# Kernel tuning notes

Measured on AMD Instinct MI355X. Metric: run time of the kernel, lower is better.

## Reference

```python
import jax, jax.numpy as jnp
import numpy as np
from jax import lax

B, G, Hh, Wn = 16, 30, 24, 862   # batch, num_group, block_len(patch_len), enc_in
PRE = G * Hh                      # 720 = configs.pre_train
RATES = (1, 2)                    # configs.dilation_rate
K = 3                             # deformable / ff kernel size


def conv2d(x, w, b, pad, dil=1):
    y = lax.conv_general_dilated(x, w, (1, 1), [(pad, pad), (pad, pad)],
                                 rhs_dilation=(dil, dil),
                                 dimension_numbers=('NCHW', 'OIHW', 'NCHW'))
    return y + b[None, :, None, None]


def bilinear_sample(x, py, px):
    # x [B,C,H,W]; py,px [B,K2,H,W] -> [B,C,K2,H,W]; zero padding outside bounds
    H, W = x.shape[2], x.shape[3]
    y0f = jnp.floor(py); x0f = jnp.floor(px)
    wy = py - y0f; wx = px - x0f
    y0 = y0f.astype(jnp.int32); x0 = x0f.astype(jnp.int32)

    def corner(yi, xi, wgt):
        m = ((yi >= 0) & (yi < H) & (xi >= 0) & (xi < W)).astype(x.dtype)
        yc = jnp.clip(yi, 0, H - 1); xc = jnp.clip(xi, 0, W - 1)
        v = jax.vmap(lambda xb, yb, xbi: xb[:, yb, xbi])(x, yc, xc)  # [B,C,K2,H,W]
        return v * (m * wgt)[:, None]

    return (corner(y0, x0, (1 - wy) * (1 - wx))
            + corner(y0, x0 + 1, (1 - wy) * wx)
            + corner(y0 + 1, x0, wy * (1 - wx))
            + corner(y0 + 1, x0 + 1, wy * wx))


def deform_conv(x, w_off, b_off, w_def, b_def, r):
    # torchvision-style deform_conv2d with 3x3 kernel, dilation r, same padding
    b, c, h, w = x.shape
    off = conv2d(x, w_off, b_off, pad=r, dil=r).reshape(b, K * K, 2, h, w)
    kg = np.stack(np.meshgrid(np.arange(K) - 1, np.arange(K) - 1, indexing='ij'), -1).reshape(-1, 2)
    py = off[:, :, 0] + jnp.arange(h, dtype=x.dtype)[None, None, :, None] \
         + jnp.asarray(kg[:, 0] * r, x.dtype)[None, :, None, None]
    px = off[:, :, 1] + jnp.arange(w, dtype=x.dtype)[None, None, None, :] \
         + jnp.asarray(kg[:, 1] * r, x.dtype)[None, :, None, None]
    sampled = bilinear_sample(x, py, px)  # [B,C,9,H,W]
    o = w_def.shape[0]
    return jnp.einsum('bikhw,oik->bohw', sampled, w_def.reshape(o, c, K * K)) \
           + b_def[None, :, None, None]


def forward(x_enc, W_bl, b_bl, W_off, b_off, W_def, b_def, W_ff, b_ff, W_proj, b_proj):
    b = x_enc.shape[0]
    # block_linear on channel(group) dim: permute(0,2,3,1) -> Linear(G,G) -> permute back
    group_inner = jnp.einsum('bghw,kg->bkhw', x_enc, W_bl) + b_bl[None, :, None, None]
    # Multi_Def_Conv: sum of deformable conv branches over dilation rates
    mul_def = deform_conv(x_enc, W_off[0], b_off[0], W_def[0], b_def[0], RATES[0])
    for ri in range(1, len(RATES)):
        mul_def = mul_def + deform_conv(x_enc, W_off[ri], b_off[ri], W_def[ri], b_def[ri], RATES[ri])
    # softmax-gated fusion
    repres = group_inner + group_inner * jax.nn.softmax(mul_def, axis=1)
    # ff = Conv2d(G,G,3,pad=1) + Dropout (identity at eval)
    repres = conv2d(repres, W_ff, b_ff, pad=1)
    all_fea = repres.reshape(b, G * Hh, Wn)          # [B, pre_train, n]
    # proj(all_fea.permute(0,2,1)).permute(0,2,1)
    return jnp.einsum('bpn,qp->bqn', all_fea, W_proj) + b_proj[None, :, None]


def setup_inputs() -> dict:
    key = jax.random.key(0)
    ks = jax.random.split(key, 6)
    R = len(RATES)
    f32 = jnp.float32
    return {
        'x_enc': jax.random.normal(ks[0], (B, G, Hh, Wn), f32),
        'W_bl': jax.random.normal(ks[1], (G, G), f32) / np.sqrt(G).astype(np.float32),
        'b_bl': jnp.zeros((G,), f32),
        'W_off': jax.random.normal(ks[2], (R, 2 * K * K, G, K, K), f32) * 0.01,
        'b_off': jnp.zeros((R, 2 * K * K), f32),
        'W_def': jax.random.normal(ks[3], (R, G, G, K, K), f32) / np.sqrt(G * K * K).astype(np.float32),
        'b_def': jnp.zeros((R, G), f32),
        'W_ff': jax.random.normal(ks[4], (G, G, K, K), f32) / np.sqrt(G * K * K).astype(np.float32),
        'b_ff': jnp.zeros((G,), f32),
        'W_proj': jax.random.normal(ks[5], (PRE, PRE), f32) / np.sqrt(PRE).astype(np.float32),
        'b_proj': jnp.zeros((PRE,), f32),
        'epoch': 0,
        'i': 0,
    }


def reference(x_enc, W_bl, b_bl, W_off, b_off, W_def, b_def, W_ff, b_ff, W_proj, b_proj, epoch, i):
    return forward(x_enc, W_bl, b_bl, W_off, b_off, W_def, b_def, W_ff, b_ff, W_proj, b_proj)
```

## Files before the change

kernel.cpp:

```cpp
#include <hip/hip_runtime.h>

#define Bz 16
#define Gc 30
#define Hs 24
#define Wd_ 862
#define HW (Hs*Wd_)
#define BHW (Bz*HW)
#define PREN 720

__device__ __forceinline__ int imin(int a,int b){return a<b?a:b;}
__device__ __forceinline__ int imax(int a,int b){return a>b?a:b;}

struct Corners { float m00,m01,m10,m11; int i00,i01,i10,i11; };

__device__ __forceinline__ Corners mk_corners(float py, float px){
  float y0f = floorf(py), x0f = floorf(px);
  float wy = py - y0f, wx = px - x0f;
  int y0 = (int)y0f, x0 = (int)x0f;
  int y1 = y0 + 1, x1 = x0 + 1;
  bool y0i = ((unsigned)y0 < (unsigned)Hs);
  bool y1i = ((unsigned)y1 < (unsigned)Hs);
  bool x0i = ((unsigned)x0 < (unsigned)Wd_);
  bool x1i = ((unsigned)x1 < (unsigned)Wd_);
  float w00=(1.f-wy)*(1.f-wx), w01=(1.f-wy)*wx, w10=wy*(1.f-wx), w11=wy*wx;
  Corners c;
  c.m00 = (y0i&&x0i)?w00:0.f; c.m01=(y0i&&x1i)?w01:0.f;
  c.m10 = (y1i&&x0i)?w10:0.f; c.m11=(y1i&&x1i)?w11:0.f;
  int y0c=imin(imax(y0,0),Hs-1), y1c=imin(imax(y1,0),Hs-1);
  int x0c=imin(imax(x0,0),Wd_-1), x1c=imin(imax(x1,0),Wd_-1);
  c.i00=y0c*Wd_+x0c; c.i01=y0c*Wd_+x1c; c.i10=y1c*Wd_+x0c; c.i11=y1c*Wd_+x1c;
  return c;
}

#define WR_TOT 36288
__global__ __launch_bounds__(256) void k_repack(
    const float* __restrict__ Woff, const float* __restrict__ Wdef,
    const float* __restrict__ Wff, float* __restrict__ wr)
{
  int i = blockIdx.x*256 + threadIdx.x;
  if (i >= WR_TOT) return;
  float v;
  if (i < 10368){
    int r = i/5184, rm = i%5184;
    int ki = rm/576, rm2 = rm%576, o = rm2>>5, c = rm2&31;
    v = (c<Gc) ? Woff[r*4860 + (o*Gc+c)*9 + ki] : 0.f;
  } else if (i < 27648){
    int j = i-10368; int r = j/8640, rm = j%8640;
    int ki = rm/960, rm2 = rm%960, o = rm2>>5, c = rm2&31;
    v = (c<Gc) ? Wdef[r*8100 + (o*Gc+c)*9 + ki] : 0.f;
  } else {
    int j = i-27648; int ki = j/960, rm2 = j%960, o = rm2>>5, c = rm2&31;
    v = (c<Gc) ? Wff[(o*Gc+c)*9 + ki] : 0.f;
  }
  wr[i] = v;
}

__global__ __launch_bounds__(256) void k_transpose(
    const float* __restrict__ x, float* __restrict__ xT)
{
  __shared__ float xs[Gc][129];
  const int b = blockIdx.z, h = blockIdx.y, w0 = blockIdx.x*128;
  for (int i = threadIdx.x; i < Gc*128; i += 256){
    int c = i >> 7, ww = i & 127;
    int wg = w0 + ww;
    xs[c][ww] = (wg < Wd_) ? x[((size_t)b*Gc + c)*HW + (size_t)h*Wd_ + wg] : 0.f;
  }
  __syncthreads();
  const int ww = threadIdx.x;
  if (ww < 128 && w0 + ww < Wd_){
    float* dst = xT + ((size_t)(b*Hs + h)*Wd_ + w0 + ww)*(size_t)Gc;
    #pragma unroll
    for (int k=0;k<15;k++)
      ((float2*)dst)[k] = make_float2(xs[2*k][ww], xs[2*k+1][ww]);
  }
}

template<int OC, int R>
__global__ __launch_bounds__(256) void k_conv3x3w(
    const float* __restrict__ x, const float* __restrict__ wrep,
    const float* __restrict__ bo, float* __restrict__ out)
{
  constexpr int TILE = 128, SW = TILE + 2*R;
  constexpr int OH = OC / 2;
  __shared__ float xs[Gc][3][SW];

  const int b = blockIdx.z, h = blockIdx.y, w0 = blockIdx.x * TILE;

  const float* xb = x + (size_t)b*Gc*HW;
  for (int i = threadIdx.x; i < Gc*3*SW; i += 256){
    int c = i/(3*SW), rm = i%(3*SW); int rr = rm/SW, ww = rm%SW;
    int hh = h + (rr-1)*R; int wg = w0 + ww - R;
    float v = 0.f;
    if ((unsigned)hh < (unsigned)Hs && (unsigned)wg < (unsigned)Wd_)
      v = xb[(size_t)c*HW + (size_t)hh*Wd_ + wg];
    xs[c][rr][ww] = v;
  }
  __syncthreads();

  const int p = threadIdx.x & 127;
  const int q = __builtin_amdgcn_readfirstlane(threadIdx.x >> 7);
  float acc[OH];
  #pragma unroll
  for (int o=0;o<OH;o++) acc[o] = 0.f;

  for (int ki = 0; ki < 9; ki++){
    const int rr = ki/3, dxx = ki%3;
    float xv[Gc];
    #pragma unroll
    for (int c=0;c<Gc;c++) xv[c] = xs[c][rr][p + dxx*R];
    const float* wk = wrep + (size_t)(ki*OC + q*OH)*32;
    #pragma unroll
    for (int o=0;o<OH;o++){
      float a = acc[o];
      #pragma unroll
      for (int c=0;c<Gc;c++) a += wk[o*32 + c]*xv[c];
      acc[o] = a;
    }
  }

  const int wpix = w0 + p;
  if (wpix < Wd_){
    float* ob_ = out + (size_t)b*OC*HW + (size_t)h*Wd_ + wpix;
    #pragma unroll
    for (int o=0;o<OH;o++){
      int oo = q*OH + o;
      ob_[(size_t)oo*HW] = acc[o] + bo[oo];
    }
  }
}

template<int R>
__global__ __launch_bounds__(256) void k_deform5(
    const float* __restrict__ xT, const float* __restrict__ off,
    const float* __restrict__ wrep,
    const float* __restrict__ bd,
    float* __restrict__ out, int first)
{
  const int nb = gridDim.x;
  const int qq = nb >> 3, rr8 = nb & 7;
  const int xcd = blockIdx.x & 7, lin = blockIdx.x >> 3;
  const int wgid = (xcd < rr8 ? xcd*(qq+1) : rr8*(qq+1) + (xcd-rr8)*qq) + lin;

  const long idx = (long)wgid*256 + threadIdx.x;
  const int b = (int)(idx / HW); const int s = (int)(idx % HW);
  const int h = s / Wd_, w = s - h*Wd_;
  const float* xTb = xT  + (size_t)b*HW*Gc;
  const float* ofb = off + (size_t)b*18*HW + s;

  float oyv[9], oxv[9];
  #pragma unroll
  for (int ki=0; ki<9; ki++){
    oyv[ki] = ofb[(size_t)(2*ki)*HW];
    oxv[ki] = ofb[(size_t)(2*ki+1)*HW];
  }

  float acc[Gc];
  #pragma unroll
  for (int o=0;o<Gc;o++) acc[o] = 0.f;

  for (int ki = 0; ki < 9; ki++){
    Corners cr = mk_corners(oyv[ki] + (float)(h + (ki/3 - 1)*R),
                            oxv[ki] + (float)(w + (ki%3 - 1)*R));
    const float2* p00 = (const float2*)(xTb + (size_t)cr.i00*Gc);
    const float2* p01 = (const float2*)(xTb + (size_t)cr.i01*Gc);
    const float2* p10 = (const float2*)(xTb + (size_t)cr.i10*Gc);
    const float2* p11 = (const float2*)(xTb + (size_t)cr.i11*Gc);
    float2 sv[15];
    #pragma unroll
    for (int k=0;k<15;k++){
      float2 a0 = p00[k], a1 = p01[k], a2 = p10[k], a3 = p11[k];
      sv[k].x = cr.m00*a0.x + cr.m01*a1.x + cr.m10*a2.x + cr.m11*a3.x;
      sv[k].y = cr.m00*a0.y + cr.m01*a1.y + cr.m10*a2.y + cr.m11*a3.y;
    }
    const float* wk = wrep + (size_t)ki*Gc*32;
    #pragma unroll
    for (int o=0;o<Gc;o++){
      float a = acc[o];
      #pragma unroll
      for (int k=0;k<15;k++){
        a += wk[o*32 + 2*k]   * sv[k].x;
        a += wk[o*32 + 2*k+1] * sv[k].y;
      }
      acc[o] = a;
    }
  }

  float* ob = out + (size_t)b*Gc*HW + s;
  if (first){
    #pragma unroll
    for (int o=0;o<Gc;o++) ob[(size_t)o*HW] = acc[o] + bd[o];
  } else {
    #pragma unroll
    for (int o=0;o<Gc;o++) ob[(size_t)o*HW] += acc[o] + bd[o];
  }
}

__global__ __launch_bounds__(256) void k_gate3(
    const float* __restrict__ x, const float* __restrict__ Wbl,
    const float* __restrict__ bbl, float* __restrict__ md)
{
  long idx = (long)blockIdx.x*256 + threadIdx.x;
  if (idx >= (long)BHW) return;
  int b = (int)(idx / HW); int s = (int)(idx % HW);
  const float* xp = x  + (size_t)b*Gc*HW + s;
  float*       mp = md + (size_t)b*Gc*HW + s;

  float xv[Gc];
  #pragma unroll
  for (int c=0;c<Gc;c++) xv[c] = xp[(size_t)c*HW];

  float gi[Gc];
  #pragma unroll
  for (int k=0;k<Gc;k++){
    float a = bbl[k];
    #pragma unroll
    for (int c=0;c<Gc;c++) a += Wbl[k*Gc + c]*xv[c];
    gi[k] = a;
  }

  float v[Gc]; float mx = -1e30f;
  #pragma unroll
  for (int c=0;c<Gc;c++){ v[c] = mp[(size_t)c*HW]; mx = fmaxf(mx, v[c]); }
  float sum = 0.f;
  #pragma unroll
  for (int c=0;c<Gc;c++){ v[c] = __expf(v[c]-mx); sum += v[c]; }
  float inv = 1.f/sum;
  #pragma unroll
  for (int c=0;c<Gc;c++) mp[(size_t)c*HW] = gi[c] + gi[c]*(v[c]*inv);
}

__global__ __launch_bounds__(256) void k_proj(
    const float* __restrict__ F, const float* __restrict__ Wp,
    const float* __restrict__ bp, float* __restrict__ out)
{
  __shared__ float As[16][68];
  __shared__ float Bs[16][64];
  const int b = blockIdx.z;
  const int q0 = blockIdx.y*64;
  const int n0 = blockIdx.x*64;
  const int tid = threadIdx.x;
  const int tm = tid >> 4, tn = tid & 15;
  const int ar = tid >> 4, ac = tid & 15;
  const int br = tid >> 6, bc = tid & 63;
  const float* Fb = F + (size_t)b*PREN*Wd_;
  float acc[4][4] = {};
  for (int k0 = 0; k0 < PREN; k0 += 16){
    #pragma unroll
    for (int i=0;i<4;i++){
      int q = q0 + ar + 16*i;
      As[ac][ar + 16*i] = (q < PREN) ? Wp[(size_t)q*PREN + k0 + ac] : 0.f;
    }
    #pragma unroll
    for (int i=0;i<4;i++){
      int p = k0 + br + 4*i;
      int n = n0 + bc;
      Bs[br + 4*i][bc] = (n < Wd_) ? Fb[(size_t)p*Wd_ + n] : 0.f;
    }
    __syncthreads();
    #pragma unroll
    for (int k=0;k<16;k++){
      float4 a4 = *(const float4*)&As[k][tm*4];
      float4 b4 = *(const float4*)&Bs[k][tn*4];
      float av[4] = {a4.x,a4.y,a4.z,a4.w};
      float bv[4] = {b4.x,b4.y,b4.z,b4.w};
      #pragma unroll
      for (int i=0;i<4;i++)
        #pragma unroll
        for (int j=0;j<4;j++) acc[i][j] += av[i]*bv[j];
    }
    __syncthreads();
  }
  #pragma unroll
  for (int i=0;i<4;i++){
    int q = q0 + tm*4 + i;
    if (q >= PREN) continue;
    float bias = bp[q];
    #pragma unroll
    for (int j=0;j<4;j++){
      int n = n0 + tn*4 + j;
      if (n < Wd_) out[((size_t)b*PREN + q)*Wd_ + n] = acc[i][j] + bias;
    }
  }
}

extern "C" void kernel_launch(void* const* d_in, const int* in_sizes, int n_in,
                              void* d_out, int out_size, void* d_ws, size_t ws_size,
                              hipStream_t stream)
{
  (void)in_sizes; (void)n_in; (void)out_size; (void)ws_size;
  const float* x    = (const float*)d_in[0];
  const float* Wbl  = (const float*)d_in[1];
  const float* bbl  = (const float*)d_in[2];
  const float* Woff = (const float*)d_in[3];
  const float* boff = (const float*)d_in[4];
  const float* Wdef = (const float*)d_in[5];
  const float* bdef = (const float*)d_in[6];
  const float* Wff  = (const float*)d_in[7];
  const float* bff  = (const float*)d_in[8];
  const float* Wp   = (const float*)d_in[9];
  const float* bp   = (const float*)d_in[10];
  float* out = (float*)d_out;

  char* ws = (char*)d_ws;
  const size_t TEN = (size_t)BHW*Gc*sizeof(float);
  float* xT   = (float*)ws;
  float* mdef = (float*)(ws + TEN);
  float* offb = (float*)d_out;
  float* wrep = (float*)((char*)d_out + (32u<<20));
  float* Fbuf = xT;

  const float* wr_off0 = wrep;
  const float* wr_off1 = wrep + 5184;
  const float* wr_def0 = wrep + 10368;
  const float* wr_def1 = wrep + 19008;
  const float* wr_ff   = wrep + 27648;

  const dim3 gconv((Wd_ + 127)/128, Hs, Bz);
  const int nblkPx = (BHW + 255)/256;

  k_repack<<<(WR_TOT+255)/256,256,0,stream>>>(Woff, Wdef, Wff, wrep);
  k_transpose<<<gconv,256,0,stream>>>(x, xT);

  k_conv3x3w<18,1><<<gconv,256,0,stream>>>(x, wr_off0, boff,      offb);
  k_deform5<1><<<nblkPx,256,0,stream>>>(xT, offb, wr_def0, bdef,      mdef, 1);
  k_conv3x3w<18,2><<<gconv,256,0,stream>>>(x, wr_off1, boff + 18, offb);
  k_deform5<2><<<nblkPx,256,0,stream>>>(xT, offb, wr_def1, bdef + 30, mdef, 0);

  k_gate3<<<nblkPx,256,0,stream>>>(x, Wbl, bbl, mdef);

  k_conv3x3w<30,1><<<gconv,256,0,stream>>>(mdef, wr_ff, bff, Fbuf);

  dim3 gp((Wd_+63)/64, (PREN+63)/64, Bz);
  k_proj<<<gp,256,0,stream>>>(Fbuf, Wp, bp, out);
}
```

Baseline: 1.514 ms.

## Run final projection GEMM on bf16 MFMA with pre-converted transposed operands

Replaces the fp32 SIMT tiled projection GEMM with a bf16 MFMA 16x16x32 kernel. Two new kernels convert the projection weight to bf16 and convert-transpose the feature tensor to bf16 in n-major layout so that K is contiguous for the MFMA fragments. The goal is to move the roughly 16x720x720x862 GEMM onto matrix cores. The trade-offs are reduced precision versus the fp32 reference, two extra conversion passes through memory, and a small 48x64 tile that is reloaded through shared memory every 32-wide K step with no prefetch.

```diff
diff --git a/kernel.cpp b/kernel.cpp
--- a/kernel.cpp
+++ b/kernel.cpp
@@ -1,4 +1,5 @@
 #include <hip/hip_runtime.h>
+#include <hip/hip_bf16.h>
 
 #define Bz 16
 #define Gc 30
@@ -8,8 +9,16 @@
 #define BHW (Bz*HW)
 #define PREN 720
 
+typedef __attribute__((ext_vector_type(8))) short bf16x8;
+typedef __attribute__((ext_vector_type(4))) float f32x4;
+
 __device__ __forceinline__ int imin(int a,int b){return a<b?a:b;}
 __device__ __forceinline__ int imax(int a,int b){return a>b?a:b;}
+
+__device__ __forceinline__ unsigned short f2bf(float f){
+  __hip_bfloat16 h = __float2bfloat16(f);
+  return *reinterpret_cast<unsigned short*>(&h);
+}
 
 struct Corners { float m00,m01,m10,m11; int i00,i01,i10,i11; };
 
@@ -229,56 +238,93 @@
   for (int c=0;c<Gc;c++) mp[(size_t)c*HW] = gi[c] + gi[c]*(v[c]*inv);
 }
 
-__global__ __launch_bounds__(256) void k_proj(
-    const float* __restrict__ F, const float* __restrict__ Wp,
+__global__ __launch_bounds__(256) void k_cvt_w(
+    const float* __restrict__ Wp, unsigned short* __restrict__ Wbf)
+{
+  int i = blockIdx.x*256 + threadIdx.x;
+  if (i < PREN*PREN) Wbf[i] = f2bf(Wp[i]);
+}
+
+__global__ __launch_bounds__(256) void k_cvtT(
+    const float* __restrict__ F, unsigned short* __restrict__ Ft)
+{
+  __shared__ float xs[48][65];
+  const int b = blockIdx.z, p0 = blockIdx.y*48, n0 = blockIdx.x*64;
+  const float* Fb = F + (size_t)b*PREN*Wd_;
+  #pragma unroll
+  for (int t=0;t<12;t++){
+    int idx = t*256 + threadIdx.x;
+    int pr = idx >> 6, nc = idx & 63;
+    xs[pr][nc] = (n0+nc < Wd_) ? Fb[(size_t)(p0+pr)*Wd_ + n0+nc] : 0.f;
+  }
+  __syncthreads();
+  unsigned short* Tb = Ft + (size_t)b*Wd_*PREN;
+  #pragma unroll
+  for (int t=0;t<6;t++){
+    int idx = t*256 + threadIdx.x;
+    int row = idx/24, cu = idx - row*24;
+    if (n0+row < Wd_){
+      unsigned int lo = f2bf(xs[cu*2][row]);
+      unsigned int hi = f2bf(xs[cu*2+1][row]);
+      ((unsigned int*)(Tb + (size_t)(n0+row)*PREN + p0))[cu] = lo | (hi<<16);
+    }
+  }
+}
+
+__global__ __launch_bounds__(256) void k_projm(
+    const unsigned short* __restrict__ Wbf,
+    const unsigned short* __restrict__ Fbt,
     const float* __restrict__ bp, float* __restrict__ out)
 {
-  __shared__ float As[16][68];
-  __shared__ float Bs[16][64];
-  const int b = blockIdx.z;
-  const int q0 = blockIdx.y*64;
-  const int n0 = blockIdx.x*64;
+  __shared__ unsigned short As[48*40];
+  __shared__ unsigned short Bs[64*40];
+  const int b = blockIdx.z, q0 = blockIdx.y*48, n0 = blockIdx.x*64;
   const int tid = threadIdx.x;
-  const int tm = tid >> 4, tn = tid & 15;
-  const int ar = tid >> 4, ac = tid & 15;
-  const int br = tid >> 6, bc = tid & 63;
-  const float* Fb = F + (size_t)b*PREN*Wd_;
-  float acc[4][4] = {};
-  for (int k0 = 0; k0 < PREN; k0 += 16){
-    #pragma unroll
-    for (int i=0;i<4;i++){
-      int q = q0 + ar + 16*i;
-      As[ac][ar + 16*i] = (q < PREN) ? Wp[(size_t)q*PREN + k0 + ac] : 0.f;
-    }
-    #pragma unroll
-    for (int i=0;i<4;i++){
-      int p = k0 + br + 4*i;
-      int n = n0 + bc;
-      Bs[br + 4*i][bc] = (n < Wd_) ? Fb[(size_t)p*Wd_ + n] : 0.f;
+  const int lane = tid & 63, wv = tid >> 6;
+  const unsigned short* Fb = Fbt + (size_t)b*Wd_*PREN;
+
+  f32x4 acc[3];
+  #pragma unroll
+  for (int rt=0;rt<3;rt++)
+    #pragma unroll
+    for (int i=0;i<4;i++) acc[rt][i] = 0.f;
+
+  for (int k0 = 0; k0 < PREN; k0 += 32){
+    #pragma unroll
+    for (int t=0;t<3;t++){
+      int idx = t*256 + tid; int row = idx >> 4, cu = idx & 15;
+      unsigned int v = 0;
+      if (k0 + cu*2 < PREN)
+        v = *(const unsigned int*)(Wbf + (size_t)(q0+row)*PREN + k0 + cu*2);
+      ((unsigned int*)As)[row*20 + cu] = v;
+    }
+    #pragma unroll
+    for (int t=0;t<4;t++){
+      int idx = t*256 + tid; int row = idx >> 4, cu = idx & 15;
+      unsigned int v = 0;
+      if ((n0+row) < Wd_ && k0 + cu*2 < PREN)
+        v = *(const unsigned int*)(Fb + (size_t)(n0+row)*PREN + k0 + cu*2);
+      ((unsigned int*)Bs)[row*20 + cu] = v;
     }
     __syncthreads();
-    #pragma unroll
-    for (int k=0;k<16;k++){
-      float4 a4 = *(const float4*)&As[k][tm*4];
-      float4 b4 = *(const float4*)&Bs[k][tn*4];
-      float av[4] = {a4.x,a4.y,a4.z,a4.w};
-      float bv[4] = {b4.x,b4.y,b4.z,b4.w};
+    bf16x8 bfr = *(const bf16x8*)(Bs + (size_t)(wv*16 + (lane&15))*40 + (lane>>4)*8);
+    #pragma unroll
+    for (int rt=0;rt<3;rt++){
+      bf16x8 afr = *(const bf16x8*)(As + (size_t)(rt*16 + (lane&15))*40 + (lane>>4)*8);
+      acc[rt] = __builtin_amdgcn_mfma_f32_16x16x32_bf16(afr, bfr, acc[rt], 0, 0, 0);
+    }
+    __syncthreads();
+  }
+
+  const int n = n0 + wv*16 + (lane&15);
+  if (n < Wd_){
+    #pragma unroll
+    for (int rt=0;rt<3;rt++){
       #pragma unroll
-      for (int i=0;i<4;i++)
-        #pragma unroll
-        for (int j=0;j<4;j++) acc[i][j] += av[i]*bv[j];
-    }
-    __syncthreads();
-  }
-  #pragma unroll
-  for (int i=0;i<4;i++){
-    int q = q0 + tm*4 + i;
-    if (q >= PREN) continue;
-    float bias = bp[q];
-    #pragma unroll
-    for (int j=0;j<4;j++){
-      int n = n0 + tn*4 + j;
-      if (n < Wd_) out[((size_t)b*PREN + q)*Wd_ + n] = acc[i][j] + bias;
+      for (int i=0;i<4;i++){
+        int q = q0 + rt*16 + (lane>>4)*4 + i;
+        out[((size_t)b*PREN + q)*Wd_ + n] = acc[rt][i] + bp[q];
+      }
     }
   }
 }
@@ -308,6 +354,8 @@
   float* offb = (float*)d_out;
   float* wrep = (float*)((char*)d_out + (32u<<20));
   float* Fbuf = xT;
+  unsigned short* Wbf  = (unsigned short*)(ws + TEN);
+  unsigned short* Fbft = (unsigned short*)(ws + TEN + (1u<<20)*2);
 
   const float* wr_off0 = wrep;
   const float* wr_off1 = wrep + 5184;
@@ -330,6 +378,10 @@
 
   k_conv3x3w<30,1><<<gconv,256,0,stream>>>(mdef, wr_ff, bff, Fbuf);
 
-  dim3 gp((Wd_+63)/64, (PREN+63)/64, Bz);
-  k_proj<<<gp,256,0,stream>>>(Fbuf, Wp, bp, out);
-}
+  k_cvt_w<<<(PREN*PREN+255)/256,256,0,stream>>>(Wp, Wbf);
+  dim3 gcv((Wd_+63)/64, PREN/48, Bz);
+  k_cvtT<<<gcv,256,0,stream>>>(Fbuf, Fbft);
+
+  dim3 gp((Wd_+63)/64, PREN/48, Bz);
+  k_projm<<<gp,256,0,stream>>>(Wbf, Fbft, bp, out);
+}
```

Result: faster. 1.352 ms (-10.7%).
